# Kernel tuning notes

Hardware: AMD Instinct MI355X
Metric: run time of the kernel (lower is better)

## Reference

```python
import jax, jax.numpy as jnp
import numpy as np

COMMITMENT_COST = 0.25
N_TOKENS = 32768
NUM_EMBEDDINGS = 8192
EMBEDDING_DIM = 256


def setup_inputs() -> dict:
    key = jax.random.key(0)
    k1, k2 = jax.random.split(key)
    z_e = jax.random.normal(k1, (N_TOKENS, EMBEDDING_DIM), dtype=jnp.float32)
    embeddings = jax.random.normal(k2, (NUM_EMBEDDINGS, EMBEDDING_DIM), dtype=jnp.float32)
    return {"z_e": z_e, "embeddings": embeddings}


def reference(z_e, embeddings):
    # Pairwise squared L2 distances: ||z||^2 - 2 z.e + ||e||^2  -> (N, K)
    z_sq = jnp.sum(z_e * z_e, axis=-1, keepdims=True)          # (N, 1)
    e_sq = jnp.sum(embeddings * embeddings, axis=-1)            # (K,)
    cross = jnp.einsum('nd,kd->nk', z_e, embeddings)            # (N, K) GEMM
    distances = z_sq - 2.0 * cross + e_sq[None, :]
    encoding_indices = jnp.argmin(distances, axis=1)            # (N,)
    z_q = embeddings[encoding_indices]                          # gather (N, D)

    sg = jax.lax.stop_gradient
    commitment_loss = jnp.mean((sg(z_e) - z_q) ** 2)
    embedding_loss = jnp.mean((z_e - sg(z_q)) ** 2)
    vq_loss = embedding_loss + COMMITMENT_COST * commitment_loss

    # straight-through estimator
    z_q_st = z_e + sg(z_q - z_e)
    return z_q_st, vq_loss, encoding_indices
```

## Files before the change

### kernel.cpp

```cpp
#include <hip/hip_runtime.h>

typedef float f32x4 __attribute__((ext_vector_type(4)));
typedef short s16x8 __attribute__((ext_vector_type(8)));

#define NT 32768
#define NK 8192
#define ND 256
#define NSP 64

static __device__ __forceinline__ ushort f2bf(float f) {
  unsigned u = __float_as_uint(f);
  unsigned r = (u + 0x7FFFu + ((u >> 16) & 1u)) >> 16;
  return (ushort)r;
}

__global__ __launch_bounds__(256) void vq_cvt(const float* __restrict__ src,
                                              ushort* __restrict__ dst) {
  size_t idx = (size_t)blockIdx.x * 256 + threadIdx.x;
  size_t n = idx >> 6;
  int dq = (int)(idx & 63) * 4;
  float4 v = *reinterpret_cast<const float4*>(src + n * ND + dq);
  float f[4] = {v.x, v.y, v.z, v.w};
  ushort h[4], l[4];
#pragma unroll
  for (int t = 0; t < 4; ++t) {
    h[t] = f2bf(f[t]);
    float hf = __uint_as_float((unsigned)h[t] << 16);
    l[t] = f2bf(f[t] - hf);
  }
  *reinterpret_cast<ushort4*>(dst + n * 512 + dq) = make_ushort4(h[0], h[1], h[2], h[3]);
  *reinterpret_cast<ushort4*>(dst + n * 512 + 256 + dq) = make_ushort4(l[0], l[1], l[2], l[3]);
}

__global__ __launch_bounds__(256) void vq_esq(const float* __restrict__ emb,
                                              float* __restrict__ esq) {
  int w = threadIdx.x >> 6, lane = threadIdx.x & 63;
  int k = blockIdx.x * 4 + w;
  const float4 e = *reinterpret_cast<const float4*>(emb + (size_t)k * ND + lane * 4);
  float s = e.x * e.x + e.y * e.y + e.z * e.z + e.w * e.w;
#pragma unroll
  for (int off = 32; off >= 1; off >>= 1) s += __shfl_down(s, off);
  if (lane == 0) esq[k] = s;
}

#define GL16(gp, lp)                                                              \
  __builtin_amdgcn_global_load_lds(                                               \
      (const __attribute__((address_space(1))) unsigned int*)(gp),                \
      (__attribute__((address_space(3))) unsigned int*)(lp), 16, 0, 0)

__global__ __launch_bounds__(256, 3) void vq_mfma(
    const ushort* __restrict__ z2, const ushort* __restrict__ e2,
    const float* __restrict__ esq, float* __restrict__ pdist,
    int* __restrict__ pidx) {
  __shared__ char smem[21504];
  ushort* ldsA = (ushort*)smem;
  ushort* ldsB = (ushort*)(smem + 8192);
  float* rdv = (float*)smem;
  unsigned char* rdc = (unsigned char*)(smem + 17408);

  const int gid = blockIdx.x;
  const int x = gid & 7, c = gid >> 3;
  const int st = x * 32 + (c >> 6);
  const int wi = c & 63;
  const int mt = (st >> 3) * 8 + (wi >> 3);
  const int nt = (st & 7) * 8 + (wi & 7);
  const int m0 = mt * 128, n0 = nt * 128;

  const int tid = threadIdx.x, lane = tid & 63, wid = tid >> 6;
  const int wr = wid >> 1, wc = wid & 1;
  const int srow = lane >> 2;
  const int sslot = (lane & 3) ^ ((lane >> 3) & 3);
  const int fr = lane & 15, g = lane >> 4;
  const int lbyte = fr * 64 + (((g ^ (fr >> 1)) & 3) << 4);

  const ushort* aBase = z2 + (size_t)(m0 + srow) * 512 + sslot * 8;
  const ushort* bBase = e2 + (size_t)(n0 + srow) * 512 + sslot * 8;

  f32x4 acc[4][4];
  const f32x4 zero = {0.f, 0.f, 0.f, 0.f};
#pragma unroll
  for (int i = 0; i < 4; ++i)
#pragma unroll
    for (int j = 0; j < 4; ++j) acc[i][j] = zero;

  for (int ks = 0; ks < 24; ++ks) {
    const int term = ks >> 3, inner = ks & 7;
    const int aoff = ((term == 2) ? 256 : 0) + inner * 32;
    const int boff = ((term == 1) ? 256 : 0) + inner * 32;
#pragma unroll
    for (int r = 0; r < 2; ++r) {
      const int ch = wid * 2 + r;
      GL16(aBase + (size_t)ch * 8192 + aoff, (char*)ldsA + ch * 1024);
      GL16(bBase + (size_t)ch * 8192 + boff, (char*)ldsB + ch * 1024);
    }
    __syncthreads();
    s16x8 af[4], bf[4];
#pragma unroll
    for (int i = 0; i < 4; ++i)
      af[i] = *reinterpret_cast<const s16x8*>((char*)ldsA + wr * 4096 + i * 1024 + lbyte);
#pragma unroll
    for (int j = 0; j < 4; ++j)
      bf[j] = *reinterpret_cast<const s16x8*>((char*)ldsB + wc * 4096 + j * 1024 + lbyte);
#pragma unroll
    for (int i = 0; i < 4; ++i)
#pragma unroll
      for (int j = 0; j < 4; ++j)
        acc[i][j] = __builtin_amdgcn_mfma_f32_16x16x32_bf16(af[i], bf[j], acc[i][j], 0, 0, 0);
    __syncthreads();
  }

  float eqv[4];
#pragma unroll
  for (int j = 0; j < 4; ++j) eqv[j] = esq[n0 + wc * 64 + j * 16 + fr];

#pragma unroll
  for (int i = 0; i < 4; ++i)
#pragma unroll
    for (int r = 0; r < 4; ++r) {
      float bv = 3.4e38f; int bc = 0;
#pragma unroll
      for (int j = 0; j < 4; ++j) {
        float dist = fmaf(-2.f, acc[i][j][r], eqv[j]);
        int cl = wc * 64 + j * 16 + fr;
        if (dist < bv) { bv = dist; bc = cl; }
      }
      int row = wr * 64 + i * 16 + g * 4 + r;
      rdv[row * 34 + wc * 16 + fr] = bv;
      rdc[row * 32 + wc * 16 + fr] = (unsigned char)bc;
    }
  __syncthreads();
  {
    const int row = tid >> 1, h = tid & 1;
    const float* pv = rdv + row * 34 + h * 16;
    const unsigned char* pc = rdc + row * 32 + h * 16;
    float bv = 3.4e38f; int bc = 128;
#pragma unroll
    for (int s = 0; s < 16; ++s) {
      float v = pv[s]; int cc = pc[s];
      if (v < bv || (v == bv && cc < bc)) { bv = v; bc = cc; }
    }
    float ov = __shfl_xor(bv, 1);
    int oc = __shfl_xor(bc, 1);
    if (ov < bv || (ov == bv && oc < bc)) { bv = ov; bc = oc; }
    if (h == 0) {
      int n = m0 + row;
      pdist[(size_t)n * NSP + nt] = bv;
      pidx[(size_t)n * NSP + nt] = n0 + bc;
    }
  }
}

__global__ __launch_bounds__(256) void vq_gather(
    const float* __restrict__ z, const float* __restrict__ emb,
    const float* __restrict__ pdist, const int* __restrict__ pidx,
    float* __restrict__ out, float* __restrict__ lpart) {
  int w = threadIdx.x >> 6, lane = threadIdx.x & 63;
  int n = blockIdx.x * 4 + w;
  float d = pdist[(size_t)n * NSP + lane];
  int ii = pidx[(size_t)n * NSP + lane];
#pragma unroll
  for (int off = 1; off < 64; off <<= 1) {
    float od = __shfl_xor(d, off);
    int oi = __shfl_xor(ii, off);
    if (od < d || (od == d && oi < ii)) { d = od; ii = oi; }
  }
  int bi = ii;
  float4 q = *reinterpret_cast<const float4*>(emb + (size_t)bi * ND + lane * 4);
  float4 zz = *reinterpret_cast<const float4*>(z + (size_t)n * ND + lane * 4);
  *reinterpret_cast<float4*>(out + (size_t)n * ND + lane * 4) = q;
  float dx = zz.x - q.x, dy = zz.y - q.y, dz = zz.z - q.z, dw = zz.w - q.w;
  float s2 = dx * dx + dy * dy + dz * dz + dw * dw;
#pragma unroll
  for (int off = 32; off >= 1; off >>= 1) s2 += __shfl_down(s2, off);
  __shared__ float ls[4];
  if (lane == 0) {
    ls[w] = s2;
    out[(size_t)NT * ND + 1 + n] = (float)bi;
  }
  __syncthreads();
  if (threadIdx.x == 0) lpart[blockIdx.x] = ls[0] + ls[1] + ls[2] + ls[3];
}

__global__ __launch_bounds__(256) void vq_finalize(const float* __restrict__ lpart,
                                                   float* __restrict__ out) {
  __shared__ float s[256];
  float acc = 0.f;
  for (int i = threadIdx.x; i < NT / 4; i += 256) acc += lpart[i];
  s[threadIdx.x] = acc;
  __syncthreads();
  for (int st = 128; st >= 1; st >>= 1) {
    if (threadIdx.x < st) s[threadIdx.x] += s[threadIdx.x + st];
    __syncthreads();
  }
  if (threadIdx.x == 0)
    out[(size_t)NT * ND] = 1.25f * s[0] / (float)((size_t)NT * ND);
}

extern "C" void kernel_launch(void* const* d_in, const int* in_sizes, int n_in,
                              void* d_out, int out_size, void* d_ws, size_t ws_size,
                              hipStream_t stream) {
  const float* z = (const float*)d_in[0];
  const float* emb = (const float*)d_in[1];
  float* out = (float*)d_out;

  float* esq = (float*)d_ws;
  ushort* z2 = (ushort*)(esq + NK);
  ushort* e2 = z2 + (size_t)NT * 512;
  float* pdist = (float*)(e2 + (size_t)NK * 512);
  int* pidx = (int*)(pdist + (size_t)NT * NSP);
  float* lpart = (float*)(pidx + (size_t)NT * NSP);

  vq_cvt<<<NT / 4, 256, 0, stream>>>(z, z2);
  vq_cvt<<<NK / 4, 256, 0, stream>>>(emb, e2);
  vq_esq<<<NK / 4, 256, 0, stream>>>(emb, esq);
  vq_mfma<<<16384, 256, 0, stream>>>(z2, e2, esq, pdist, pidx);
  vq_gather<<<NT / 4, 256, 0, stream>>>(z, emb, pdist, pidx, out, lpart);
  vq_finalize<<<1, 256, 0, stream>>>(lpart, out);
}
```

Before: 491.2 us.

## Enlarge MFMA tiles to 256x256 with double-buffered async LDS pipeline

Restructures the distance GEMM kernel to use 512-thread blocks computing 256x256 tiles with K-chunks of 64, staged through a 128KB double-buffered LDS via global_load_lds. Loads for the next K-steps are interleaved with MFMA groups under raw s_barrier and explicit vmcnt waits, and MFMA sections raise wave priority. The larger tile halves the partial-argmin count per row, giving the gather kernel less to reduce. The trade-off is much heavier LDS and register use, which limits occupancy, and a hand-tuned waitcnt schedule that is fragile.

```diff
diff --git a/kernel.cpp b/kernel.cpp
--- a/kernel.cpp
+++ b/kernel.cpp
@@ -6,7 +6,8 @@
 #define NT 32768
 #define NK 8192
 #define ND 256
-#define NSP 64
+#define NSP 32
+#define NKT 12
 
 static __device__ __forceinline__ ushort f2bf(float f) {
   unsigned u = __float_as_uint(f);
@@ -48,73 +49,131 @@
       (const __attribute__((address_space(1))) unsigned int*)(gp),                \
       (__attribute__((address_space(3))) unsigned int*)(lp), 16, 0, 0)
 
-__global__ __launch_bounds__(256, 3) void vq_mfma(
+#define BAR()                                                                     \
+  do {                                                                            \
+    asm volatile("" ::: "memory");                                                \
+    __builtin_amdgcn_s_barrier();                                                 \
+    asm volatile("" ::: "memory");                                                \
+  } while (0)
+
+__device__ __forceinline__ int koffA(int kt) { return ((kt >= 8) ? 256 : 0) + (kt & 3) * 64; }
+__device__ __forceinline__ int koffB(int kt) { return ((kt >= 4 && kt < 8) ? 256 : 0) + (kt & 3) * 64; }
+
+__global__ __launch_bounds__(512, 2) void vq_mfma(
     const ushort* __restrict__ z2, const ushort* __restrict__ e2,
     const float* __restrict__ esq, float* __restrict__ pdist,
     int* __restrict__ pidx) {
-  __shared__ char smem[21504];
-  ushort* ldsA = (ushort*)smem;
-  ushort* ldsB = (ushort*)(smem + 8192);
-  float* rdv = (float*)smem;
-  unsigned char* rdc = (unsigned char*)(smem + 17408);
+  __shared__ __align__(16) char smem[131072];
+  char* ldsA = smem;
+  char* ldsB = smem + 65536;
 
   const int gid = blockIdx.x;
   const int x = gid & 7, c = gid >> 3;
-  const int st = x * 32 + (c >> 6);
-  const int wi = c & 63;
-  const int mt = (st >> 3) * 8 + (wi >> 3);
-  const int nt = (st & 7) * 8 + (wi & 7);
-  const int m0 = mt * 128, n0 = nt * 128;
+  const int mt = x * 16 + (c >> 5);
+  const int nt = c & 31;
+  const int m0 = mt * 256, n0 = nt * 256;
 
   const int tid = threadIdx.x, lane = tid & 63, wid = tid >> 6;
-  const int wr = wid >> 1, wc = wid & 1;
-  const int srow = lane >> 2;
-  const int sslot = (lane & 3) ^ ((lane >> 3) & 3);
+  const int wr = wid >> 2, wc = wid & 3;
   const int fr = lane & 15, g = lane >> 4;
-  const int lbyte = fr * 64 + (((g ^ (fr >> 1)) & 3) << 4);
-
-  const ushort* aBase = z2 + (size_t)(m0 + srow) * 512 + sslot * 8;
-  const ushort* bBase = e2 + (size_t)(n0 + srow) * 512 + sslot * 8;
-
-  f32x4 acc[4][4];
+
+  const ushort* aBase = z2 + (size_t)(m0 + (tid >> 2)) * 512 + (tid & 3) * 8;
+  const ushort* bBase = e2 + (size_t)(n0 + (tid >> 2)) * 512 + (tid & 3) * 8;
+
+#define STAGE_A(kt, kh)                                                           \
+  do {                                                                            \
+    const ushort* _g = aBase + koffA(kt) + (kh) * 32;                             \
+    char* _l = ldsA + (((kt) & 1) << 15) + ((kh) << 14) + tid * 16;               \
+    GL16(_g, _l);                                                                 \
+    GL16(_g + 65536, _l + 8192);                                                  \
+  } while (0)
+#define STAGE_B(kt, kh)                                                           \
+  do {                                                                            \
+    const ushort* _g = bBase + koffB(kt) + (kh) * 32;                             \
+    char* _l = ldsB + (((kt) & 1) << 15) + ((kh) << 14) + tid * 16;               \
+    GL16(_g, _l);                                                                 \
+    GL16(_g + 65536, _l + 8192);                                                  \
+  } while (0)
+
+  const int aro = (wr * 128 + fr) * 64 + g * 16;
+  const int bro = (wc * 64 + fr) * 64 + g * 16;
+
+  f32x4 acc[8][4];
   const f32x4 zero = {0.f, 0.f, 0.f, 0.f};
 #pragma unroll
-  for (int i = 0; i < 4; ++i)
+  for (int i = 0; i < 8; ++i)
 #pragma unroll
     for (int j = 0; j < 4; ++j) acc[i][j] = zero;
 
-  for (int ks = 0; ks < 24; ++ks) {
-    const int term = ks >> 3, inner = ks & 7;
-    const int aoff = ((term == 2) ? 256 : 0) + inner * 32;
-    const int boff = ((term == 1) ? 256 : 0) + inner * 32;
-#pragma unroll
-    for (int r = 0; r < 2; ++r) {
-      const int ch = wid * 2 + r;
-      GL16(aBase + (size_t)ch * 8192 + aoff, (char*)ldsA + ch * 1024);
-      GL16(bBase + (size_t)ch * 8192 + boff, (char*)ldsB + ch * 1024);
-    }
-    __syncthreads();
-    s16x8 af[4], bf[4];
-#pragma unroll
-    for (int i = 0; i < 4; ++i)
-      af[i] = *reinterpret_cast<const s16x8*>((char*)ldsA + wr * 4096 + i * 1024 + lbyte);
-#pragma unroll
-    for (int j = 0; j < 4; ++j)
-      bf[j] = *reinterpret_cast<const s16x8*>((char*)ldsB + wc * 4096 + j * 1024 + lbyte);
-#pragma unroll
-    for (int i = 0; i < 4; ++i)
-#pragma unroll
-      for (int j = 0; j < 4; ++j)
-        acc[i][j] = __builtin_amdgcn_mfma_f32_16x16x32_bf16(af[i], bf[j], acc[i][j], 0, 0, 0);
-    __syncthreads();
+  STAGE_A(0, 0); STAGE_B(0, 0); STAGE_A(0, 1); STAGE_B(0, 1);
+  STAGE_A(1, 0); STAGE_B(1, 0); STAGE_A(1, 1);
+  asm volatile("s_waitcnt vmcnt(6)" ::: "memory");
+  BAR();
+
+#define MMACC(J0, J1)                                                             \
+  do {                                                                            \
+    __builtin_amdgcn_s_setprio(1);                                                \
+    _Pragma("unroll") for (int i = 0; i < 8; ++i) {                               \
+      acc[i][J0] = __builtin_amdgcn_mfma_f32_16x16x32_bf16(af[i], b0, acc[i][J0], 0, 0, 0); \
+      acc[i][J1] = __builtin_amdgcn_mfma_f32_16x16x32_bf16(af[i], b1, acc[i][J1], 0, 0, 0); \
+    }                                                                             \
+    __builtin_amdgcn_s_setprio(0);                                                \
+  } while (0)
+
+#pragma unroll 2
+  for (int kt = 0; kt < NKT; ++kt) {
+    const int bufo = (kt & 1) << 15;
+    const char* pa = ldsA + bufo + aro;
+    const char* pb = ldsB + bufo + bro;
+    s16x8 af[8], b0, b1;
+
+    b0 = *(const s16x8*)(pb);
+    b1 = *(const s16x8*)(pb + 1024);
+#pragma unroll
+    for (int i = 0; i < 8; ++i) af[i] = *(const s16x8*)(pa + i * 1024);
+    if (kt + 1 < NKT) STAGE_B(kt + 1, 1);
+    BAR();
+    MMACC(0, 1);
+    BAR();
+
+    b0 = *(const s16x8*)(pb + 2048);
+    b1 = *(const s16x8*)(pb + 3072);
+    if (kt + 2 < NKT) STAGE_A(kt + 2, 0);
+    BAR();
+    MMACC(2, 3);
+    BAR();
+
+    b0 = *(const s16x8*)(pb + 16384);
+    b1 = *(const s16x8*)(pb + 16384 + 1024);
+#pragma unroll
+    for (int i = 0; i < 8; ++i) af[i] = *(const s16x8*)(pa + 16384 + i * 1024);
+    if (kt + 2 < NKT) STAGE_B(kt + 2, 0);
+    BAR();
+    MMACC(0, 1);
+    BAR();
+
+    b0 = *(const s16x8*)(pb + 16384 + 2048);
+    b1 = *(const s16x8*)(pb + 16384 + 3072);
+    if (kt + 2 < NKT) STAGE_A(kt + 2, 1);
+    BAR();
+    MMACC(2, 3);
+    if (kt == NKT - 2) {
+      asm volatile("s_waitcnt vmcnt(0)" ::: "memory");
+    } else {
+      asm volatile("s_waitcnt vmcnt(6)" ::: "memory");
+    }
+    BAR();
   }
 
   float eqv[4];
 #pragma unroll
   for (int j = 0; j < 4; ++j) eqv[j] = esq[n0 + wc * 64 + j * 16 + fr];
 
-#pragma unroll
-  for (int i = 0; i < 4; ++i)
+  float* rdv = (float*)smem;
+  unsigned char* rdc = (unsigned char*)(smem + 98304);
+
+#pragma unroll
+  for (int i = 0; i < 8; ++i)
 #pragma unroll
     for (int r = 0; r < 4; ++r) {
       float bv = 3.4e38f; int bc = 0;
@@ -124,18 +183,18 @@
         int cl = wc * 64 + j * 16 + fr;
         if (dist < bv) { bv = dist; bc = cl; }
       }
-      int row = wr * 64 + i * 16 + g * 4 + r;
-      rdv[row * 34 + wc * 16 + fr] = bv;
-      rdc[row * 32 + wc * 16 + fr] = (unsigned char)bc;
-    }
-  __syncthreads();
+      int row = wr * 128 + i * 16 + g * 4 + r;
+      rdv[row * 67 + wc * 16 + fr] = bv;
+      rdc[row * 64 + wc * 16 + fr] = (unsigned char)bc;
+    }
+  BAR();
   {
     const int row = tid >> 1, h = tid & 1;
-    const float* pv = rdv + row * 34 + h * 16;
-    const unsigned char* pc = rdc + row * 32 + h * 16;
-    float bv = 3.4e38f; int bc = 128;
-#pragma unroll
-    for (int s = 0; s < 16; ++s) {
+    const float* pv = rdv + row * 67 + h * 32;
+    const unsigned char* pc = rdc + row * 64 + h * 32;
+    float bv = 3.4e38f; int bc = 256;
+#pragma unroll
+    for (int s = 0; s < 32; ++s) {
       float v = pv[s]; int cc = pc[s];
       if (v < bv || (v == bv && cc < bc)) { bv = v; bc = cc; }
     }
@@ -156,10 +215,11 @@
     float* __restrict__ out, float* __restrict__ lpart) {
   int w = threadIdx.x >> 6, lane = threadIdx.x & 63;
   int n = blockIdx.x * 4 + w;
-  float d = pdist[(size_t)n * NSP + lane];
-  int ii = pidx[(size_t)n * NSP + lane];
-#pragma unroll
-  for (int off = 1; off < 64; off <<= 1) {
+  int p = lane & (NSP - 1);
+  float d = pdist[(size_t)n * NSP + p];
+  int ii = pidx[(size_t)n * NSP + p];
+#pragma unroll
+  for (int off = 1; off < NSP; off <<= 1) {
     float od = __shfl_xor(d, off);
     int oi = __shfl_xor(ii, off);
     if (od < d || (od == d && oi < ii)) { d = od; ii = oi; }
@@ -213,7 +273,7 @@
   vq_cvt<<<NT / 4, 256, 0, stream>>>(z, z2);
   vq_cvt<<<NK / 4, 256, 0, stream>>>(emb, e2);
   vq_esq<<<NK / 4, 256, 0, stream>>>(emb, esq);
-  vq_mfma<<<16384, 256, 0, stream>>>(z2, e2, esq, pdist, pidx);
+  vq_mfma<<<4096, 512, 0, stream>>>(z2, e2, esq, pdist, pidx);
   vq_gather<<<NT / 4, 256, 0, stream>>>(z, emb, pdist, pidx, out, lpart);
   vq_finalize<<<1, 256, 0, stream>>>(lpart, out);
 }
```

Measured after the change: 482.8 us. About the same (-1.7%).

## Use 256x256 tiles with 32x32 MFMA loading operands directly from global

Applied to the files above, without the earlier changes.

Tiles grow from 128x128 per 256-thread block to 256x256 per 512-thread block. The LDS staging and per-step barriers are removed: each wave loads its bf16 A/B fragments straight from global memory into registers and issues 32x32x16 MFMAs. The argmin reduction now runs through cross-lane shuffles before a small LDS merge, and the number of partial results per token drops from 64 to 32. This cuts barrier and LDS overhead and doubles arithmetic intensity per block, but it relies on cache reuse of the uncoalesced direct global loads and adds register pressure.

```diff
diff --git a/kernel.cpp b/kernel.cpp
--- a/kernel.cpp
+++ b/kernel.cpp
@@ -1,12 +1,13 @@
 #include <hip/hip_runtime.h>
 
 typedef float f32x4 __attribute__((ext_vector_type(4)));
+typedef float f32x16 __attribute__((ext_vector_type(16)));
 typedef short s16x8 __attribute__((ext_vector_type(8)));
 
 #define NT 32768
 #define NK 8192
 #define ND 256
-#define NSP 64
+#define NSP 32
 
 static __device__ __forceinline__ ushort f2bf(float f) {
   unsigned u = __float_as_uint(f);
@@ -43,110 +44,97 @@
   if (lane == 0) esq[k] = s;
 }
 
-#define GL16(gp, lp)                                                              \
-  __builtin_amdgcn_global_load_lds(                                               \
-      (const __attribute__((address_space(1))) unsigned int*)(gp),                \
-      (__attribute__((address_space(3))) unsigned int*)(lp), 16, 0, 0)
-
-__global__ __launch_bounds__(256, 3) void vq_mfma(
+__global__ __launch_bounds__(512, 2) void vq_mfma(
     const ushort* __restrict__ z2, const ushort* __restrict__ e2,
     const float* __restrict__ esq, float* __restrict__ pdist,
     int* __restrict__ pidx) {
-  __shared__ char smem[21504];
-  ushort* ldsA = (ushort*)smem;
-  ushort* ldsB = (ushort*)(smem + 8192);
-  float* rdv = (float*)smem;
-  unsigned char* rdc = (unsigned char*)(smem + 17408);
-
   const int gid = blockIdx.x;
   const int x = gid & 7, c = gid >> 3;
-  const int st = x * 32 + (c >> 6);
+  const int S = x * 8 + (c >> 6);
   const int wi = c & 63;
-  const int mt = (st >> 3) * 8 + (wi >> 3);
-  const int nt = (st & 7) * 8 + (wi & 7);
-  const int m0 = mt * 128, n0 = nt * 128;
+  const int mt = (S >> 2) * 8 + (wi >> 3);
+  const int nt = (S & 3) * 8 + (wi & 7);
+  const int m0 = mt * 256, n0 = nt * 256;
 
   const int tid = threadIdx.x, lane = tid & 63, wid = tid >> 6;
-  const int wr = wid >> 1, wc = wid & 1;
-  const int srow = lane >> 2;
-  const int sslot = (lane & 3) ^ ((lane >> 3) & 3);
-  const int fr = lane & 15, g = lane >> 4;
-  const int lbyte = fr * 64 + (((g ^ (fr >> 1)) & 3) << 4);
-
-  const ushort* aBase = z2 + (size_t)(m0 + srow) * 512 + sslot * 8;
-  const ushort* bBase = e2 + (size_t)(n0 + srow) * 512 + sslot * 8;
-
-  f32x4 acc[4][4];
-  const f32x4 zero = {0.f, 0.f, 0.f, 0.f};
-#pragma unroll
-  for (int i = 0; i < 4; ++i)
-#pragma unroll
-    for (int j = 0; j < 4; ++j) acc[i][j] = zero;
-
-  for (int ks = 0; ks < 24; ++ks) {
-    const int term = ks >> 3, inner = ks & 7;
-    const int aoff = ((term == 2) ? 256 : 0) + inner * 32;
-    const int boff = ((term == 1) ? 256 : 0) + inner * 32;
-#pragma unroll
-    for (int r = 0; r < 2; ++r) {
-      const int ch = wid * 2 + r;
-      GL16(aBase + (size_t)ch * 8192 + aoff, (char*)ldsA + ch * 1024);
-      GL16(bBase + (size_t)ch * 8192 + boff, (char*)ldsB + ch * 1024);
+  const int wr = wid >> 2, wc = wid & 3;
+  const int ll = lane & 31, h = lane >> 5;
+
+  const ushort* aP[4];
+  const ushort* bP[2];
+#pragma unroll
+  for (int mi = 0; mi < 4; ++mi)
+    aP[mi] = z2 + (size_t)(m0 + wr * 128 + mi * 32 + ll) * 512 + h * 8;
+#pragma unroll
+  for (int ni = 0; ni < 2; ++ni)
+    bP[ni] = e2 + (size_t)(n0 + wc * 64 + ni * 32 + ll) * 512 + h * 8;
+
+  f32x16 acc[4][2];
+#pragma unroll
+  for (int mi = 0; mi < 4; ++mi)
+#pragma unroll
+    for (int ni = 0; ni < 2; ++ni)
+#pragma unroll
+      for (int r = 0; r < 16; ++r) acc[mi][ni][r] = 0.f;
+
+  for (int term = 0; term < 3; ++term) {
+    const int aoff = (term == 2) ? 256 : 0;
+    const int boff = (term == 1) ? 256 : 0;
+#pragma unroll 4
+    for (int inner = 0; inner < 16; ++inner) {
+      const int ae = aoff + inner * 16;
+      const int be = boff + inner * 16;
+      s16x8 a[4], b[2];
+#pragma unroll
+      for (int ni = 0; ni < 2; ++ni) b[ni] = *(const s16x8*)(bP[ni] + be);
+#pragma unroll
+      for (int mi = 0; mi < 4; ++mi) a[mi] = *(const s16x8*)(aP[mi] + ae);
+#pragma unroll
+      for (int mi = 0; mi < 4; ++mi)
+#pragma unroll
+        for (int ni = 0; ni < 2; ++ni)
+          acc[mi][ni] = __builtin_amdgcn_mfma_f32_32x32x16_bf16(a[mi], b[ni], acc[mi][ni], 0, 0, 0);
     }
-    __syncthreads();
-    s16x8 af[4], bf[4];
-#pragma unroll
-    for (int i = 0; i < 4; ++i)
-      af[i] = *reinterpret_cast<const s16x8*>((char*)ldsA + wr * 4096 + i * 1024 + lbyte);
-#pragma unroll
-    for (int j = 0; j < 4; ++j)
-      bf[j] = *reinterpret_cast<const s16x8*>((char*)ldsB + wc * 4096 + j * 1024 + lbyte);
-#pragma unroll
-    for (int i = 0; i < 4; ++i)
-#pragma unroll
-      for (int j = 0; j < 4; ++j)
-        acc[i][j] = __builtin_amdgcn_mfma_f32_16x16x32_bf16(af[i], bf[j], acc[i][j], 0, 0, 0);
-    __syncthreads();
-  }
-
-  float eqv[4];
-#pragma unroll
-  for (int j = 0; j < 4; ++j) eqv[j] = esq[n0 + wc * 64 + j * 16 + fr];
-
-#pragma unroll
-  for (int i = 0; i < 4; ++i)
-#pragma unroll
-    for (int r = 0; r < 4; ++r) {
+  }
+
+  __shared__ float rdv[256][4];
+  __shared__ int rdi[256][4];
+
+  float eqv[2];
+#pragma unroll
+  for (int ni = 0; ni < 2; ++ni) eqv[ni] = esq[n0 + wc * 64 + ni * 32 + ll];
+
+#pragma unroll
+  for (int mi = 0; mi < 4; ++mi)
+#pragma unroll
+    for (int reg = 0; reg < 16; ++reg) {
       float bv = 3.4e38f; int bc = 0;
 #pragma unroll
-      for (int j = 0; j < 4; ++j) {
-        float dist = fmaf(-2.f, acc[i][j][r], eqv[j]);
-        int cl = wc * 64 + j * 16 + fr;
+      for (int ni = 0; ni < 2; ++ni) {
+        float dist = fmaf(-2.f, acc[mi][ni][reg], eqv[ni]);
+        int cl = wc * 64 + ni * 32 + ll;
         if (dist < bv) { bv = dist; bc = cl; }
       }
-      int row = wr * 64 + i * 16 + g * 4 + r;
-      rdv[row * 34 + wc * 16 + fr] = bv;
-      rdc[row * 32 + wc * 16 + fr] = (unsigned char)bc;
+#pragma unroll
+      for (int off = 1; off < 32; off <<= 1) {
+        float ov = __shfl_xor(bv, off);
+        int oc = __shfl_xor(bc, off);
+        if (ov < bv || (ov == bv && oc < bc)) { bv = ov; bc = oc; }
+      }
+      int row = wr * 128 + mi * 32 + (reg & 3) + 8 * (reg >> 2) + 4 * h;
+      if (ll == 0) { rdv[row][wc] = bv; rdi[row][wc] = bc; }
     }
   __syncthreads();
-  {
-    const int row = tid >> 1, h = tid & 1;
-    const float* pv = rdv + row * 34 + h * 16;
-    const unsigned char* pc = rdc + row * 32 + h * 16;
-    float bv = 3.4e38f; int bc = 128;
-#pragma unroll
-    for (int s = 0; s < 16; ++s) {
-      float v = pv[s]; int cc = pc[s];
+  if (tid < 256) {
+    float bv = rdv[tid][0]; int bc = rdi[tid][0];
+#pragma unroll
+    for (int w = 1; w < 4; ++w) {
+      float v = rdv[tid][w]; int cc = rdi[tid][w];
       if (v < bv || (v == bv && cc < bc)) { bv = v; bc = cc; }
     }
-    float ov = __shfl_xor(bv, 1);
-    int oc = __shfl_xor(bc, 1);
-    if (ov < bv || (ov == bv && oc < bc)) { bv = ov; bc = oc; }
-    if (h == 0) {
-      int n = m0 + row;
-      pdist[(size_t)n * NSP + nt] = bv;
-      pidx[(size_t)n * NSP + nt] = n0 + bc;
-    }
+    int n = m0 + tid;
+    pdist[(size_t)n * NSP + nt] = bv;
+    pidx[(size_t)n * NSP + nt] = n0 + bc;
   }
 }
 
@@ -156,10 +144,11 @@
     float* __restrict__ out, float* __restrict__ lpart) {
   int w = threadIdx.x >> 6, lane = threadIdx.x & 63;
   int n = blockIdx.x * 4 + w;
-  float d = pdist[(size_t)n * NSP + lane];
-  int ii = pidx[(size_t)n * NSP + lane];
-#pragma unroll
-  for (int off = 1; off < 64; off <<= 1) {
+  int p = lane & (NSP - 1);
+  float d = pdist[(size_t)n * NSP + p];
+  int ii = pidx[(size_t)n * NSP + p];
+#pragma unroll
+  for (int off = 1; off < NSP; off <<= 1) {
     float od = __shfl_xor(d, off);
     int oi = __shfl_xor(ii, off);
     if (od < d || (od == d && oi < ii)) { d = od; ii = oi; }
@@ -213,7 +202,7 @@
   vq_cvt<<<NT / 4, 256, 0, stream>>>(z, z2);
   vq_cvt<<<NK / 4, 256, 0, stream>>>(emb, e2);
   vq_esq<<<NK / 4, 256, 0, stream>>>(emb, esq);
-  vq_mfma<<<16384, 256, 0, stream>>>(z2, e2, esq, pdist, pidx);
+  vq_mfma<<<4096, 512, 0, stream>>>(z2, e2, esq, pdist, pidx);
   vq_gather<<<NT / 4, 256, 0, stream>>>(z, emb, pdist, pidx, out, lpart);
   vq_finalize<<<1, 256, 0, stream>>>(lpart, out);
 }
```

After: 1.582 ms. 3.22x slower.
